# Optimization experiments

Hardware: AMD Instinct MI355X
Metric: run time of the kernel (lower is better)

## Reference

```python
import jax, jax.numpy as jnp
import numpy as np

DIM = 128
HEADS = 2
SR = 8
LN_EPS = 1e-5


def setup_inputs() -> dict:
    key = jax.random.key(0)
    ks = jax.random.split(key, 8)
    B, H, W, C = 8, 128, 128, DIM
    s = 0.02
    return {
        "x": jax.random.normal(ks[0], (B, H * W, C), jnp.float32),
        "h": H,
        "w": W,
        "Wq": jax.random.normal(ks[1], (C, C), jnp.float32) * s,
        "bq": jnp.zeros((C,), jnp.float32),
        "Wkv": jax.random.normal(ks[2], (2 * C, C), jnp.float32) * s,
        "bkv": jnp.zeros((2 * C,), jnp.float32),
        "Wp": jax.random.normal(ks[3], (C, C), jnp.float32) * s,
        "bp": jnp.zeros((C,), jnp.float32),
        "Wsr": jax.random.normal(ks[4], (C, C, SR, SR), jnp.float32) * s,  # OIHW
        "bsr": jnp.zeros((C,), jnp.float32),
        "gamma": jnp.ones((C,), jnp.float32),
        "beta": jnp.zeros((C,), jnp.float32),
    }


def reference(x, h, w, Wq, bq, Wkv, bkv, Wp, bp, Wsr, bsr, gamma, beta):
    b, n, c = x.shape
    hd = c // HEADS
    scale = hd ** -0.5
    # q: [b, heads, n, hd]
    q = (jnp.einsum('bnc,oc->bno', x, Wq) + bq).reshape(b, n, HEADS, hd).transpose(0, 2, 1, 3)
    # spatial reduction of k/v source: conv stride SR, then LayerNorm
    x_img = x.reshape(b, h, w, c).transpose(0, 3, 1, 2)  # NCHW
    xr = jax.lax.conv_general_dilated(
        x_img, Wsr, window_strides=(SR, SR), padding='VALID',
        dimension_numbers=('NCHW', 'OIHW', 'NCHW')) + bsr[None, :, None, None]
    xr = xr.reshape(b, c, -1).transpose(0, 2, 1)  # [b, m, c], m = (h/SR)*(w/SR)
    mu = jnp.mean(xr, axis=-1, keepdims=True)
    var = jnp.var(xr, axis=-1, keepdims=True)
    xr = (xr - mu) / jnp.sqrt(var + LN_EPS) * gamma + beta
    # k, v: [b, heads, m, hd]
    kv = jnp.einsum('bmc,oc->bmo', xr, Wkv) + bkv
    m = kv.shape[1]
    kv = kv.reshape(b, m, 2, HEADS, hd).transpose(2, 0, 3, 1, 4)
    k, v = kv[0], kv[1]
    attn = jax.nn.softmax(jnp.einsum('bhnd,bhmd->bhnm', q, k) * scale, axis=-1)
    out = jnp.einsum('bhnm,bhmd->bhnd', attn, v).transpose(0, 2, 1, 3).reshape(b, n, c)
    return jnp.einsum('bnc,oc->bno', out, Wp) + bp
```

## Files before the change

### kernel.cpp

```cpp
#include <hip/hip_runtime.h>
#include <stdint.h>

typedef __attribute__((ext_vector_type(8))) short bf16x8;
typedef __attribute__((ext_vector_type(4))) float f32x4;

#define MFMA16(A, B, C) __builtin_amdgcn_mfma_f32_16x16x32_bf16(A, B, C, 0, 0, 0)

#define LGKM_GUARD() do { asm volatile("s_waitcnt lgkmcnt(0)" ::: "memory"); \
                          __builtin_amdgcn_sched_barrier(0); } while (0)

static __device__ __forceinline__ unsigned short f2bf(float f) {
  uint32_t u = __float_as_uint(f);
  u = (u + 0x7fffu + ((u >> 16) & 1u)) >> 16;
  return (unsigned short)u;
}

static __device__ __forceinline__ bf16x8 pack8(float4 a, float4 b) {
  bf16x8 r;
  r[0] = (short)f2bf(a.x); r[1] = (short)f2bf(a.y);
  r[2] = (short)f2bf(a.z); r[3] = (short)f2bf(a.w);
  r[4] = (short)f2bf(b.x); r[5] = (short)f2bf(b.y);
  r[6] = (short)f2bf(b.z); r[7] = (short)f2bf(b.w);
  return r;
}

__global__ __launch_bounds__(256) void prep_kernel(
    const float* __restrict__ Wq, const float* __restrict__ Wkv,
    const float* __restrict__ Wp, const float* __restrict__ Wsr,
    unsigned short* __restrict__ Wq2, unsigned short* __restrict__ Wkv2,
    unsigned short* __restrict__ Wp2, unsigned short* __restrict__ W2sr) {
  const int bid = blockIdx.x;
  const int tid = threadIdx.x;
  if (bid < 64) {
    int t = bid * 256 + tid;
    int o = t >> 7, c = t & 127;
    const float4* wp = (const float4*)(Wsr + (size_t)t * 64);
#pragma unroll
    for (int s4 = 0; s4 < 16; ++s4) {
      float4 v = wp[s4];
#pragma unroll
      for (int e = 0; e < 4; ++e) {
        int s = s4 * 4 + e;
        float f = (e == 0) ? v.x : (e == 1) ? v.y : (e == 2) ? v.z : v.w;
        W2sr[(size_t)((s * 4 + (c >> 5)) * 128 + o) * 32 + (c & 31)] = f2bf(f);
      }
    }
    return;
  }
  int t = (bid - 64) * 256 + tid;
  if (t < 16384) {
    int o = t >> 7, c = t & 127;
    Wq2[((c >> 5) * 128 + o) * 32 + (c & 31)] = f2bf(Wq[t]);
  } else if (t < 32768) {
    int u = t - 16384;
    int o = u >> 7, c = u & 127;
    Wp2[((c >> 5) * 128 + o) * 32 + (c & 31)] = f2bf(Wp[u]);
  } else {
    int u = t - 32768;
    int o = u >> 7, c = u & 127;
    Wkv2[((c >> 5) * 256 + o) * 32 + (c & 31)] = f2bf(Wkv[u]);
  }
}

__global__ __launch_bounds__(256, 2) void conv_split_kernel(
    const float* __restrict__ x, const unsigned short* __restrict__ W2sr,
    float* __restrict__ scratch) {
  const int tid = threadIdx.x;
  const int wave = tid >> 6, l = tid & 63, lg = l >> 4, lr = l & 15;
  const int pt = blockIdx.x;
  const int ks = blockIdx.y;
  const int b = pt >> 4, ii = pt & 15;

  __shared__ __align__(16) unsigned short Xc[2][16384];

  const float* src = x + (size_t)b * 2097152 + (size_t)(ii * 8 + ks * 2) * 16384;
#pragma unroll
  for (int it = 0; it < 32; ++it) {
    int f = it * 1024 + tid * 4;
    float4 v = *(const float4*)(src + f);
    int row = f >> 14, o = f & 16383;
    int byteoff = (o * 2) ^ (((o >> 10) & 7) << 4);
    ushort4 h;
    h.x = f2bf(v.x); h.y = f2bf(v.y); h.z = f2bf(v.z); h.w = f2bf(v.w);
    *(ushort4*)((char*)&Xc[row][0] + byteoff) = h;
  }
  __syncthreads();

  const f32x4 zr = {0.f, 0.f, 0.f, 0.f};
  f32x4 acc[8];
#pragma unroll
  for (int ct = 0; ct < 8; ++ct) acc[ct] = zr;

  for (int kt = 0; kt < 16; ++kt) {
    const int k = ks * 2048 + wave * 512 + kt * 32;
    const int s = k >> 7, c0t = (k >> 5) & 3;
    const int kw = s & 7, yl = (s >> 3) & 1;
    int o_r = (lr * 8 + kw) * 128 + c0t * 32 + lg * 8;
    int byteoff = (o_r * 2) ^ ((lr & 7) << 4);
    bf16x8 af = *(const bf16x8*)((const char*)&Xc[yl][0] + byteoff);
    const unsigned short* wb = W2sr + (size_t)(k >> 5) * 4096;
#pragma unroll
    for (int ct = 0; ct < 8; ++ct) {
      bf16x8 bfr = *(const bf16x8*)(wb + (ct * 16 + lr) * 32 + lg * 8);
      acc[ct] = MFMA16(af, bfr, acc[ct]);
    }
  }

#pragma unroll
  for (int ct = 0; ct < 8; ++ct)
#pragma unroll
    for (int r = 0; r < 4; ++r)
      scratch[((size_t)((ks * 4 + wave) * 2048 + pt * 16 + lg * 4 + r)) * 128 + ct * 16 + lr] = acc[ct][r];
}

__global__ __launch_bounds__(256, 2) void ln_kv_kernel(
    const float* __restrict__ scratch, const float* __restrict__ bsr,
    const float* __restrict__ gamma, const float* __restrict__ beta,
    const unsigned short* __restrict__ Wkv2, const float* __restrict__ bkv,
    unsigned short* __restrict__ K2, unsigned short* __restrict__ V2) {
  const int tid = threadIdx.x;
  const int wave = tid >> 6, l = tid & 63, lg = l >> 4, lr = l & 15;
  const int blk = blockIdx.x;

  __shared__ unsigned short lns[16][136];

  {
    const int row = tid >> 4, c0 = (tid & 15) * 8;
    const int p = blk * 16 + row;
    float vals[8];
#pragma unroll
    for (int cc = 0; cc < 8; ++cc) vals[cc] = bsr[c0 + cc];
#pragma unroll
    for (int ksp = 0; ksp < 16; ++ksp) {
      const float4* sp = (const float4*)(scratch + ((size_t)(ksp * 2048 + p)) * 128 + c0);
      float4 a = sp[0], bb = sp[1];
      vals[0] += a.x; vals[1] += a.y; vals[2] += a.z; vals[3] += a.w;
      vals[4] += bb.x; vals[5] += bb.y; vals[6] += bb.z; vals[7] += bb.w;
    }
    float s1 = 0.f, s2 = 0.f;
#pragma unroll
    for (int cc = 0; cc < 8; ++cc) { s1 += vals[cc]; s2 += vals[cc] * vals[cc]; }
#pragma unroll
    for (int msk = 1; msk < 16; msk <<= 1) { s1 += __shfl_xor(s1, msk); s2 += __shfl_xor(s2, msk); }
    float mean = s1 * (1.f / 128.f);
    float var = s2 * (1.f / 128.f) - mean * mean;
    float rstd = rsqrtf(var + 1e-5f);
#pragma unroll
    for (int cc = 0; cc < 8; ++cc) {
      int c = c0 + cc;
      lns[row][c] = f2bf((vals[cc] - mean) * rstd * gamma[c] + beta[c]);
    }
  }
  __syncthreads();

  const f32x4 zr = {0.f, 0.f, 0.f, 0.f};
  f32x4 kv[4];
#pragma unroll
  for (int q = 0; q < 4; ++q) kv[q] = zr;
#pragma unroll
  for (int kt = 0; kt < 4; ++kt) {
    bf16x8 af = *(const bf16x8*)(&lns[lr][kt * 32 + lg * 8]);
#pragma unroll
    for (int q = 0; q < 4; ++q) {
      bf16x8 bfr = *(const bf16x8*)(Wkv2 + (kt * 256 + (wave * 4 + q) * 16 + lr) * 32 + lg * 8);
      kv[q] = MFMA16(af, bfr, kv[q]);
    }
  }
#pragma unroll
  for (int q = 0; q < 4; ++q)
#pragma unroll
    for (int r = 0; r < 4; ++r) {
      int o2 = (wave * 4 + q) * 16 + lr;
      int mrow = lg * 4 + r;
      int pp = blk * 16 + mrow;
      int bb = pp >> 8, mm = pp & 255;
      float val = kv[q][r] + bkv[o2];
      unsigned short hv = f2bf(val);
      if (o2 < 128) {
        int h = o2 >> 6, d = o2 & 63;
        K2[((size_t)((bb * 2 + h) * 2 + (d >> 5)) * 256 + mm) * 32 + (d & 31)] = hv;
      } else {
        int o3 = o2 - 128, h = o3 >> 6, d = o3 & 63;
        V2[((size_t)((bb * 2 + h) * 8 + (mm >> 5)) * 64 + d) * 32 + (mm & 31)] = hv;
      }
    }
}

__global__ __launch_bounds__(256, 3) void attn_kernel(
    const float* __restrict__ x, const float* __restrict__ bq, const float* __restrict__ bp,
    const unsigned short* __restrict__ Wq2, const unsigned short* __restrict__ Wp2,
    const unsigned short* __restrict__ K2, const unsigned short* __restrict__ V2,
    float* __restrict__ out) {
  const int tid = threadIdx.x;
  const int wave = tid >> 6, l = tid & 63, lg = l >> 4, lr = l & 15;
  const int b = blockIdx.y;
  const int n0 = blockIdx.x * 64 + wave * 16;

  __shared__ __align__(16) unsigned short XQ[4][16 * 136];
  __shared__ __align__(16) unsigned short PS[4][16 * 264];

  unsigned short* Xs = &XQ[wave][0];
  unsigned short* Ps = &PS[wave][0];

  const f32x4 zr = {0.f, 0.f, 0.f, 0.f};

  {
    const float* src = x + ((size_t)b * 16384 + n0) * 128;
#pragma unroll
    for (int q = 0; q < 8; ++q) {
      int f = q * 256 + l * 4;
      float4 v = *(const float4*)(src + f);
      int row = f >> 7, col = f & 127;
      ushort4 h;
      h.x = f2bf(v.x); h.y = f2bf(v.y); h.z = f2bf(v.z); h.w = f2bf(v.w);
      *(ushort4*)(Xs + row * 136 + col) = h;
    }
  }
  LGKM_GUARD();

  {
    bf16x8 af[4];
#pragma unroll
    for (int kt = 0; kt < 4; ++kt)
      af[kt] = *(const bf16x8*)(Xs + lr * 136 + kt * 32 + lg * 8);
    LGKM_GUARD();
    f32x4 qa[8];
#pragma unroll
    for (int ct = 0; ct < 8; ++ct) qa[ct] = zr;
#pragma unroll
    for (int kt = 0; kt < 4; ++kt)
#pragma unroll
      for (int ct = 0; ct < 8; ++ct) {
        bf16x8 bfr = *(const bf16x8*)(Wq2 + (kt * 128 + ct * 16 + lr) * 32 + lg * 8);
        qa[ct] = MFMA16(af[kt], bfr, qa[ct]);
      }
#pragma unroll
    for (int ct = 0; ct < 8; ++ct)
#pragma unroll
      for (int r = 0; r < 4; ++r)
        Xs[(lg * 4 + r) * 136 + ct * 16 + lr] = f2bf((qa[ct][r] + bq[ct * 16 + lr]) * 0.125f);
  }

  f32x4 oacc[2][4];
#pragma unroll
  for (int h2 = 0; h2 < 2; ++h2)
#pragma unroll
    for (int dt = 0; dt < 4; ++dt) oacc[h2][dt] = zr;

  for (int h = 0; h < 2; ++h) {
    f32x4 sacc[16];
#pragma unroll
    for (int mt = 0; mt < 16; ++mt) sacc[mt] = zr;
#pragma unroll
    for (int d0 = 0; d0 < 64; d0 += 32) {
      const unsigned short* kbase = K2 + (size_t)((b * 2 + h) * 2 + (d0 >> 5)) * 8192;
      bf16x8 qf = *(const bf16x8*)(Xs + lr * 136 + h * 64 + d0 + lg * 8);
#pragma unroll
      for (int mt = 0; mt < 16; ++mt) {
        bf16x8 kf = *(const bf16x8*)(kbase + (mt * 16 + lr) * 32 + lg * 8);
        sacc[mt] = MFMA16(kf, qf, sacc[mt]);
      }
    }
    float mx = -1e30f;
#pragma unroll
    for (int mt = 0; mt < 16; ++mt)
#pragma unroll
      for (int r = 0; r < 4; ++r) mx = fmaxf(mx, sacc[mt][r]);
    mx = fmaxf(mx, __shfl_xor(mx, 16));
    mx = fmaxf(mx, __shfl_xor(mx, 32));
    float sum = 0.f;
#pragma unroll
    for (int mt = 0; mt < 16; ++mt)
#pragma unroll
      for (int r = 0; r < 4; ++r) {
        float pv = __expf(sacc[mt][r] - mx);
        sacc[mt][r] = pv; sum += pv;
      }
    sum += __shfl_xor(sum, 16);
    sum += __shfl_xor(sum, 32);
    float inv = 1.f / sum;
    if (h == 1) LGKM_GUARD();
#pragma unroll
    for (int mt = 0; mt < 16; ++mt) {
      unsigned int w0 = (unsigned int)f2bf(sacc[mt][0] * inv) | ((unsigned int)f2bf(sacc[mt][1] * inv) << 16);
      unsigned int w1 = (unsigned int)f2bf(sacc[mt][2] * inv) | ((unsigned int)f2bf(sacc[mt][3] * inv) << 16);
      uint2 pw; pw.x = w0; pw.y = w1;
      *(uint2*)(Ps + lr * 264 + mt * 16 + lg * 4) = pw;
    }

#pragma unroll
    for (int ki = 0; ki < 8; ++ki) {
      const unsigned short* vbase = V2 + (size_t)((b * 2 + h) * 8 + ki) * 2048;
      bf16x8 pf = *(const bf16x8*)(Ps + lr * 264 + ki * 32 + lg * 8);
#pragma unroll
      for (int dt = 0; dt < 4; ++dt) {
        bf16x8 vf = *(const bf16x8*)(vbase + (dt * 16 + lr) * 32 + lg * 8);
        oacc[h][dt] = MFMA16(pf, vf, oacc[h][dt]);
      }
    }
  }

  LGKM_GUARD();
#pragma unroll
  for (int h = 0; h < 2; ++h)
#pragma unroll
    for (int dt = 0; dt < 4; ++dt)
#pragma unroll
      for (int r = 0; r < 4; ++r)
        Ps[(lg * 4 + r) * 136 + h * 64 + dt * 16 + lr] = f2bf(oacc[h][dt][r]);

  bf16x8 af2[4];
#pragma unroll
  for (int kt = 0; kt < 4; ++kt)
    af2[kt] = *(const bf16x8*)(Ps + lr * 136 + kt * 32 + lg * 8);
  LGKM_GUARD();
  f32x4 yacc[8];
#pragma unroll
  for (int ct = 0; ct < 8; ++ct) yacc[ct] = zr;
#pragma unroll
  for (int kt = 0; kt < 4; ++kt)
#pragma unroll
    for (int ct = 0; ct < 8; ++ct) {
      bf16x8 bfr = *(const bf16x8*)(Wp2 + (kt * 128 + ct * 16 + lr) * 32 + lg * 8);
      yacc[ct] = MFMA16(af2[kt], bfr, yacc[ct]);
    }

  float* Osf = (float*)Ps;
#pragma unroll
  for (int ct = 0; ct < 8; ++ct)
#pragma unroll
    for (int r = 0; r < 4; ++r)
      Osf[(lg * 4 + r) * 132 + ct * 16 + lr] = yacc[ct][r] + bp[ct * 16 + lr];

  {
    float* dst = out + ((size_t)b * 16384 + n0) * 128;
#pragma unroll
    for (int q = 0; q < 8; ++q) {
      int f = q * 256 + l * 4;
      int row = f >> 7, col = f & 127;
      float4 v = *(const float4*)(Osf + row * 132 + col);
      *(float4*)(dst + f) = v;
    }
  }
}

extern "C" void kernel_launch(void* const* d_in, const int* in_sizes, int n_in,
                              void* d_out, int out_size, void* d_ws, size_t ws_size,
                              hipStream_t stream) {
  const float* x = (const float*)d_in[0];
  const float* Wq = (const float*)d_in[3];
  const float* bq = (const float*)d_in[4];
  const float* Wkv = (const float*)d_in[5];
  const float* bkv = (const float*)d_in[6];
  const float* Wp = (const float*)d_in[7];
  const float* bp = (const float*)d_in[8];
  const float* Wsr = (const float*)d_in[9];
  const float* bsr = (const float*)d_in[10];
  const float* gamma = (const float*)d_in[11];
  const float* beta = (const float*)d_in[12];
  float* out = (float*)d_out;

  unsigned short* ws = (unsigned short*)d_ws;
  unsigned short* Wq2 = ws;
  unsigned short* Wp2 = ws + 16384;
  unsigned short* Wkv2 = ws + 32768;
  unsigned short* W2sr = ws + 65536;
  unsigned short* K2 = ws + 1114112;
  unsigned short* V2 = ws + 1376256;
  float* scratch = (float*)(ws + 1638400);

  prep_kernel<<<320, 256, 0, stream>>>(Wq, Wkv, Wp, Wsr, Wq2, Wkv2, Wp2, W2sr);
  conv_split_kernel<<<dim3(128, 4), 256, 0, stream>>>(x, W2sr, scratch);
  ln_kv_kernel<<<128, 256, 0, stream>>>(scratch, bsr, gamma, beta, Wkv2, bkv, K2, V2);
  attn_kernel<<<dim3(256, 8), 256, 0, stream>>>(x, bq, bp, Wq2, Wp2, K2, V2, out);
}
```

Measured before the change: 321.7 us.

## Split Q projection into separate kernel, fold log2e scale, use exp2 and packed bf16 conversion

Moves the Q projection out of the attention kernel into its own kernel that writes bf16 Q, pre-scaled by scale*log2(e), to workspace in MFMA fragment layout. The attention kernel then loads Q fragments directly, uses exp2f instead of __expf, and raises the occupancy hint from 3 to 4 blocks per CU. It also swaps the hand-written bf16 rounding for the HIP intrinsics, including a packed two-value conversion. The trade is an extra launch plus a 32MB bf16 Q write and read through global memory, in exchange for lower register and LDS pressure in the attention kernel.

```diff
diff --git a/kernel.cpp b/kernel.cpp
--- a/kernel.cpp
+++ b/kernel.cpp
@@ -1,4 +1,5 @@
 #include <hip/hip_runtime.h>
+#include <hip/hip_bf16.h>
 #include <stdint.h>
 
 typedef __attribute__((ext_vector_type(8))) short bf16x8;
@@ -9,19 +10,17 @@
 #define LGKM_GUARD() do { asm volatile("s_waitcnt lgkmcnt(0)" ::: "memory"); \
                           __builtin_amdgcn_sched_barrier(0); } while (0)
 
-static __device__ __forceinline__ unsigned short f2bf(float f) {
-  uint32_t u = __float_as_uint(f);
-  u = (u + 0x7fffu + ((u >> 16) & 1u)) >> 16;
-  return (unsigned short)u;
-}
-
-static __device__ __forceinline__ bf16x8 pack8(float4 a, float4 b) {
-  bf16x8 r;
-  r[0] = (short)f2bf(a.x); r[1] = (short)f2bf(a.y);
-  r[2] = (short)f2bf(a.z); r[3] = (short)f2bf(a.w);
-  r[4] = (short)f2bf(b.x); r[5] = (short)f2bf(b.y);
-  r[6] = (short)f2bf(b.z); r[7] = (short)f2bf(b.w);
-  return r;
+#define QSCL 0.1803368801111204f
+
+static __device__ __forceinline__ unsigned short bfr(float f) {
+  __hip_bfloat16 h = __float2bfloat16(f);
+  return *reinterpret_cast<unsigned short*>(&h);
+}
+
+static __device__ __forceinline__ unsigned int pk2(float a, float b) {
+  float2 t; t.x = a; t.y = b;
+  __hip_bfloat162 h = __float22bfloat162_rn(t);
+  return *reinterpret_cast<unsigned int*>(&h);
 }
 
 __global__ __launch_bounds__(256) void prep_kernel(
@@ -42,7 +41,7 @@
       for (int e = 0; e < 4; ++e) {
         int s = s4 * 4 + e;
         float f = (e == 0) ? v.x : (e == 1) ? v.y : (e == 2) ? v.z : v.w;
-        W2sr[(size_t)((s * 4 + (c >> 5)) * 128 + o) * 32 + (c & 31)] = f2bf(f);
+        W2sr[(size_t)((s * 4 + (c >> 5)) * 128 + o) * 32 + (c & 31)] = bfr(f);
       }
     }
     return;
@@ -50,15 +49,15 @@
   int t = (bid - 64) * 256 + tid;
   if (t < 16384) {
     int o = t >> 7, c = t & 127;
-    Wq2[((c >> 5) * 128 + o) * 32 + (c & 31)] = f2bf(Wq[t]);
+    Wq2[((c >> 5) * 128 + o) * 32 + (c & 31)] = bfr(Wq[t]);
   } else if (t < 32768) {
     int u = t - 16384;
     int o = u >> 7, c = u & 127;
-    Wp2[((c >> 5) * 128 + o) * 32 + (c & 31)] = f2bf(Wp[u]);
+    Wp2[((c >> 5) * 128 + o) * 32 + (c & 31)] = bfr(Wp[u]);
   } else {
     int u = t - 32768;
     int o = u >> 7, c = u & 127;
-    Wkv2[((c >> 5) * 256 + o) * 32 + (c & 31)] = f2bf(Wkv[u]);
+    Wkv2[((c >> 5) * 256 + o) * 32 + (c & 31)] = bfr(Wkv[u]);
   }
 }
 
@@ -81,7 +80,7 @@
     int row = f >> 14, o = f & 16383;
     int byteoff = (o * 2) ^ (((o >> 10) & 7) << 4);
     ushort4 h;
-    h.x = f2bf(v.x); h.y = f2bf(v.y); h.z = f2bf(v.z); h.w = f2bf(v.w);
+    h.x = bfr(v.x); h.y = bfr(v.y); h.z = bfr(v.z); h.w = bfr(v.w);
     *(ushort4*)((char*)&Xc[row][0] + byteoff) = h;
   }
   __syncthreads();
@@ -101,8 +100,8 @@
     const unsigned short* wb = W2sr + (size_t)(k >> 5) * 4096;
 #pragma unroll
     for (int ct = 0; ct < 8; ++ct) {
-      bf16x8 bfr = *(const bf16x8*)(wb + (ct * 16 + lr) * 32 + lg * 8);
-      acc[ct] = MFMA16(af, bfr, acc[ct]);
+      bf16x8 bfrg = *(const bf16x8*)(wb + (ct * 16 + lr) * 32 + lg * 8);
+      acc[ct] = MFMA16(af, bfrg, acc[ct]);
     }
   }
 
@@ -148,7 +147,7 @@
 #pragma unroll
     for (int cc = 0; cc < 8; ++cc) {
       int c = c0 + cc;
-      lns[row][c] = f2bf((vals[cc] - mean) * rstd * gamma[c] + beta[c]);
+      lns[row][c] = bfr((vals[cc] - mean) * rstd * gamma[c] + beta[c]);
     }
   }
   __syncthreads();
@@ -162,8 +161,8 @@
     bf16x8 af = *(const bf16x8*)(&lns[lr][kt * 32 + lg * 8]);
 #pragma unroll
     for (int q = 0; q < 4; ++q) {
-      bf16x8 bfr = *(const bf16x8*)(Wkv2 + (kt * 256 + (wave * 4 + q) * 16 + lr) * 32 + lg * 8);
-      kv[q] = MFMA16(af, bfr, kv[q]);
+      bf16x8 bfrg = *(const bf16x8*)(Wkv2 + (kt * 256 + (wave * 4 + q) * 16 + lr) * 32 + lg * 8);
+      kv[q] = MFMA16(af, bfrg, kv[q]);
     }
   }
 #pragma unroll
@@ -171,11 +170,10 @@
 #pragma unroll
     for (int r = 0; r < 4; ++r) {
       int o2 = (wave * 4 + q) * 16 + lr;
-      int mrow = lg * 4 + r;
-      int pp = blk * 16 + mrow;
+      int pp = blk * 16 + lg * 4 + r;
       int bb = pp >> 8, mm = pp & 255;
       float val = kv[q][r] + bkv[o2];
-      unsigned short hv = f2bf(val);
+      unsigned short hv = bfr(val);
       if (o2 < 128) {
         int h = o2 >> 6, d = o2 & 63;
         K2[((size_t)((bb * 2 + h) * 2 + (d >> 5)) * 256 + mm) * 32 + (d & 31)] = hv;
@@ -186,79 +184,96 @@
     }
 }
 
-__global__ __launch_bounds__(256, 3) void attn_kernel(
-    const float* __restrict__ x, const float* __restrict__ bq, const float* __restrict__ bp,
-    const unsigned short* __restrict__ Wq2, const unsigned short* __restrict__ Wp2,
+__global__ __launch_bounds__(256, 4) void qproj_kernel(
+    const float* __restrict__ x, const float* __restrict__ bq,
+    const unsigned short* __restrict__ Wq2, unsigned short* __restrict__ Qf) {
+  const int tid = threadIdx.x;
+  const int wave = tid >> 6, l = tid & 63, lg = l >> 4, lr = l & 15;
+  const int b = blockIdx.y;
+  const int nt = blockIdx.x * 4 + wave;
+  const int n0 = nt * 16;
+
+  __shared__ __align__(16) unsigned short XQ[4][16 * 136];
+  unsigned short* Xs = &XQ[wave][0];
+
+  const float* src = x + ((size_t)b * 16384 + n0) * 128;
+#pragma unroll
+  for (int q = 0; q < 8; ++q) {
+    int f = q * 256 + l * 4;
+    float4 v = *(const float4*)(src + f);
+    int row = f >> 7, col = f & 127;
+    ushort4 h;
+    h.x = bfr(v.x); h.y = bfr(v.y); h.z = bfr(v.z); h.w = bfr(v.w);
+    *(ushort4*)(Xs + row * 136 + col) = h;
+  }
+  LGKM_GUARD();
+
+  bf16x8 af[4];
+#pragma unroll
+  for (int kt = 0; kt < 4; ++kt)
+    af[kt] = *(const bf16x8*)(Xs + lr * 136 + kt * 32 + lg * 8);
+  LGKM_GUARD();
+
+  const f32x4 zr = {0.f, 0.f, 0.f, 0.f};
+  f32x4 qa[8];
+#pragma unroll
+  for (int ct = 0; ct < 8; ++ct) qa[ct] = zr;
+#pragma unroll
+  for (int kt = 0; kt < 4; ++kt)
+#pragma unroll
+    for (int ct = 0; ct < 8; ++ct) {
+      bf16x8 bfrg = *(const bf16x8*)(Wq2 + (kt * 128 + ct * 16 + lr) * 32 + lg * 8);
+      qa[ct] = MFMA16(af[kt], bfrg, qa[ct]);
+    }
+#pragma unroll
+  for (int ct = 0; ct < 8; ++ct)
+#pragma unroll
+    for (int r = 0; r < 4; ++r)
+      Xs[(lg * 4 + r) * 136 + ct * 16 + lr] = bfr((qa[ct][r] + bq[ct * 16 + lr]) * QSCL);
+  LGKM_GUARD();
+
+  unsigned short* qdst = Qf + ((size_t)(b * 1024 + nt) * 4) * 512 + lr * 32 + lg * 8;
+#pragma unroll
+  for (int t = 0; t < 4; ++t) {
+    bf16x8 qv = *(const bf16x8*)(Xs + lr * 136 + t * 32 + lg * 8);
+    *(bf16x8*)(qdst + t * 512) = qv;
+  }
+}
+
+__global__ __launch_bounds__(256, 4) void attn_kernel(
+    const unsigned short* __restrict__ Qf, const float* __restrict__ bp,
+    const unsigned short* __restrict__ Wp2,
     const unsigned short* __restrict__ K2, const unsigned short* __restrict__ V2,
     float* __restrict__ out) {
   const int tid = threadIdx.x;
   const int wave = tid >> 6, l = tid & 63, lg = l >> 4, lr = l & 15;
   const int b = blockIdx.y;
-  const int n0 = blockIdx.x * 64 + wave * 16;
-
-  __shared__ __align__(16) unsigned short XQ[4][16 * 136];
+  const int nt = blockIdx.x * 4 + wave;
+
   __shared__ __align__(16) unsigned short PS[4][16 * 264];
-
-  unsigned short* Xs = &XQ[wave][0];
   unsigned short* Ps = &PS[wave][0];
 
   const f32x4 zr = {0.f, 0.f, 0.f, 0.f};
-
-  {
-    const float* src = x + ((size_t)b * 16384 + n0) * 128;
-#pragma unroll
-    for (int q = 0; q < 8; ++q) {
-      int f = q * 256 + l * 4;
-      float4 v = *(const float4*)(src + f);
-      int row = f >> 7, col = f & 127;
-      ushort4 h;
-      h.x = f2bf(v.x); h.y = f2bf(v.y); h.z = f2bf(v.z); h.w = f2bf(v.w);
-      *(ushort4*)(Xs + row * 136 + col) = h;
-    }
-  }
-  LGKM_GUARD();
-
-  {
-    bf16x8 af[4];
-#pragma unroll
-    for (int kt = 0; kt < 4; ++kt)
-      af[kt] = *(const bf16x8*)(Xs + lr * 136 + kt * 32 + lg * 8);
-    LGKM_GUARD();
-    f32x4 qa[8];
-#pragma unroll
-    for (int ct = 0; ct < 8; ++ct) qa[ct] = zr;
-#pragma unroll
-    for (int kt = 0; kt < 4; ++kt)
-#pragma unroll
-      for (int ct = 0; ct < 8; ++ct) {
-        bf16x8 bfr = *(const bf16x8*)(Wq2 + (kt * 128 + ct * 16 + lr) * 32 + lg * 8);
-        qa[ct] = MFMA16(af[kt], bfr, qa[ct]);
-      }
-#pragma unroll
-    for (int ct = 0; ct < 8; ++ct)
-#pragma unroll
-      for (int r = 0; r < 4; ++r)
-        Xs[(lg * 4 + r) * 136 + ct * 16 + lr] = f2bf((qa[ct][r] + bq[ct * 16 + lr]) * 0.125f);
-  }
-
   f32x4 oacc[2][4];
 #pragma unroll
   for (int h2 = 0; h2 < 2; ++h2)
 #pragma unroll
     for (int dt = 0; dt < 4; ++dt) oacc[h2][dt] = zr;
+
+  const unsigned short* qbase = Qf + ((size_t)(b * 1024 + nt) * 4) * 512 + lr * 32 + lg * 8;
 
   for (int h = 0; h < 2; ++h) {
     f32x4 sacc[16];
 #pragma unroll
     for (int mt = 0; mt < 16; ++mt) sacc[mt] = zr;
 #pragma unroll
-    for (int d0 = 0; d0 < 64; d0 += 32) {
-      const unsigned short* kbase = K2 + (size_t)((b * 2 + h) * 2 + (d0 >> 5)) * 8192;
-      bf16x8 qf = *(const bf16x8*)(Xs + lr * 136 + h * 64 + d0 + lg * 8);
+    for (int d0i = 0; d0i < 2; ++d0i) {
+      bf16x8 qfv = *(const bf16x8*)(qbase + (h * 2 + d0i) * 512);
+      const unsigned short* kbase = K2 + (size_t)((b * 2 + h) * 2 + d0i) * 8192;
 #pragma unroll
       for (int mt = 0; mt < 16; ++mt) {
         bf16x8 kf = *(const bf16x8*)(kbase + (mt * 16 + lr) * 32 + lg * 8);
-        sacc[mt] = MFMA16(kf, qf, sacc[mt]);
+        sacc[mt] = MFMA16(kf, qfv, sacc[mt]);
       }
     }
     float mx = -1e30f;
@@ -273,7 +288,7 @@
     for (int mt = 0; mt < 16; ++mt)
 #pragma unroll
       for (int r = 0; r < 4; ++r) {
-        float pv = __expf(sacc[mt][r] - mx);
+        float pv = exp2f(sacc[mt][r] - mx);
         sacc[mt][r] = pv; sum += pv;
       }
     sum += __shfl_xor(sum, 16);
@@ -282,9 +297,9 @@
     if (h == 1) LGKM_GUARD();
 #pragma unroll
     for (int mt = 0; mt < 16; ++mt) {
-      unsigned int w0 = (unsigned int)f2bf(sacc[mt][0] * inv) | ((unsigned int)f2bf(sacc[mt][1] * inv) << 16);
-      unsigned int w1 = (unsigned int)f2bf(sacc[mt][2] * inv) | ((unsigned int)f2bf(sacc[mt][3] * inv) << 16);
-      uint2 pw; pw.x = w0; pw.y = w1;
+      uint2 pw;
+      pw.x = pk2(sacc[mt][0] * inv, sacc[mt][1] * inv);
+      pw.y = pk2(sacc[mt][2] * inv, sacc[mt][3] * inv);
       *(uint2*)(Ps + lr * 264 + mt * 16 + lg * 4) = pw;
     }
 
@@ -307,13 +322,15 @@
     for (int dt = 0; dt < 4; ++dt)
 #pragma unroll
       for (int r = 0; r < 4; ++r)
-        Ps[(lg * 4 + r) * 136 + h * 64 + dt * 16 + lr] = f2bf(oacc[h][dt][r]);
+        Ps[(lg * 4 + r) * 136 + h * 64 + dt * 16 + lr] = bfr(oacc[h][dt][r]);
+  LGKM_GUARD();
 
   bf16x8 af2[4];
 #pragma unroll
   for (int kt = 0; kt < 4; ++kt)
     af2[kt] = *(const bf16x8*)(Ps + lr * 136 + kt * 32 + lg * 8);
   LGKM_GUARD();
+
   f32x4 yacc[8];
 #pragma unroll
   for (int ct = 0; ct < 8; ++ct) yacc[ct] = zr;
@@ -321,8 +338,8 @@
   for (int kt = 0; kt < 4; ++kt)
 #pragma unroll
     for (int ct = 0; ct < 8; ++ct) {
-      bf16x8 bfr = *(const bf16x8*)(Wp2 + (kt * 128 + ct * 16 + lr) * 32 + lg * 8);
-      yacc[ct] = MFMA16(af2[kt], bfr, yacc[ct]);
+      bf16x8 bfrg = *(const bf16x8*)(Wp2 + (kt * 128 + ct * 16 + lr) * 32 + lg * 8);
+      yacc[ct] = MFMA16(af2[kt], bfrg, yacc[ct]);
     }
 
   float* Osf = (float*)Ps;
@@ -331,9 +348,10 @@
 #pragma unroll
     for (int r = 0; r < 4; ++r)
       Osf[(lg * 4 + r) * 132 + ct * 16 + lr] = yacc[ct][r] + bp[ct * 16 + lr];
+  LGKM_GUARD();
 
   {
-    float* dst = out + ((size_t)b * 16384 + n0) * 128;
+    float* dst = out + ((size_t)b * 16384 + nt * 16) * 128;
 #pragma unroll
     for (int q = 0; q < 8; ++q) {
       int f = q * 256 + l * 4;
@@ -367,10 +385,12 @@
   unsigned short* W2sr = ws + 65536;
   unsigned short* K2 = ws + 1114112;
   unsigned short* V2 = ws + 1376256;
-  float* scratch = (float*)(ws + 1638400);
+  unsigned short* Qf = ws + 1638400;
+  float* scratch = (float*)(ws + 18415616);
 
   prep_kernel<<<320, 256, 0, stream>>>(Wq, Wkv, Wp, Wsr, Wq2, Wkv2, Wp2, W2sr);
   conv_split_kernel<<<dim3(128, 4), 256, 0, stream>>>(x, W2sr, scratch);
   ln_kv_kernel<<<128, 256, 0, stream>>>(scratch, bsr, gamma, beta, Wkv2, bkv, K2, V2);
-  attn_kernel<<<dim3(256, 8), 256, 0, stream>>>(x, bq, bp, Wq2, Wp2, K2, V2, out);
-}
+  qproj_kernel<<<dim3(256, 8), 256, 0, stream>>>(x, bq, Wq2, Qf);
+  attn_kernel<<<dim3(256, 8), 256, 0, stream>>>(Qf, bp, Wp2, K2, V2, out);
+}
```

Result: faster. 281.8 us (-12.4%).
